# Optimization experiments

Hardware: AMD Instinct MI355X
Metric: run time of the kernel (lower is better)

The kernel has to match this reference:

```python
import jax, jax.numpy as jnp
import numpy as np

B, C, L = 32, 64, 2048
FREQ = L // 2 + 1            # 1025
BAND_SIZES = [341, 341, 343]  # freq//3, freq//3, remainder


def setup_inputs() -> dict:
    key = jax.random.key(0)
    k = jax.random.split(key, 6)
    X = jax.random.normal(k[0], (B, C, L), dtype=jnp.float32)
    A0 = jax.random.normal(k[1], (BAND_SIZES[0], BAND_SIZES[0]), dtype=jnp.float32)
    A1 = jax.random.normal(k[2], (BAND_SIZES[1], BAND_SIZES[1]), dtype=jnp.float32)
    A2 = jax.random.normal(k[3], (BAND_SIZES[2], BAND_SIZES[2]), dtype=jnp.float32)
    fusion_weights = jnp.ones((3,), dtype=jnp.float32)
    # Gumbel(0,1) noise for the 2-way gumbel-softmax over each (b, i, j) entry
    gumbel_noise = jax.random.gumbel(k[4], (B, C, C, 2), dtype=jnp.float32)
    return {"X": X, "A0": A0, "A1": A1, "A2": A2,
            "fusion_weights": fusion_weights, "gumbel_noise": gumbel_noise}


def _band_dist(band, A):
    # band: (b, c, s), A: (s, s). dist[b,i,j] = ||A (band_i - band_j)||^2
    # Gram trick: ||y_i - y_j||^2 = q_i + q_j - 2 y_i . y_j, y = band @ A^T
    Y = jnp.einsum('ds,bcs->bcd', A, band)          # (b, c, s)
    G = jnp.einsum('bid,bjd->bij', Y, Y)            # (b, c, c)
    q = jnp.einsum('bid,bid->bi', Y, Y)             # (b, c)
    dist = q[:, :, None] + q[:, None, :] - 2.0 * G
    return jnp.maximum(dist, 0.0)                   # guard fp round-off


def reference(X, A0, A1, A2, fusion_weights, gumbel_noise):
    XF = jnp.abs(jnp.fft.rfft(X, axis=-1))          # (b, c, FREQ)
    s0, s1, s2 = BAND_SIZES
    bands = (XF[..., :s0], XF[..., s0:s0 + s1], XF[..., s0 + s1:])
    As = (A0, A1, A2)
    dists = jnp.stack([_band_dist(b_, A_) for b_, A_ in zip(bands, As)], axis=-1)  # (b,c,c,3)
    w = jax.nn.softmax(fusion_weights)
    dist = jnp.einsum('bijk,k->bij', dists, w)      # (b, c, c)

    exp_dist = 1.0 / (dist + 1e-10)
    eye = jnp.eye(C, dtype=exp_dist.dtype)
    mask = 1.0 - eye
    exp_dist = exp_dist * mask
    exp_max = jax.lax.stop_gradient(jnp.max(exp_dist, axis=-1, keepdims=True))
    p = exp_dist / exp_max
    p = (p * mask + eye) * 0.99                     # probs in (0, 0.99]

    # Bernoulli via 2-class gumbel-softmax (hard, tau=1, straight-through)
    logits = jnp.stack([jnp.log(p / (1.0 - p)), jnp.log((1.0 - p) / p)], axis=-1)  # (b,c,c,2)
    y = logits + gumbel_noise
    y_soft = jax.nn.softmax(y, axis=-1)
    y_hard = jax.nn.one_hot(jnp.argmax(y, axis=-1), 2, dtype=y_soft.dtype)
    sample = (y_hard - jax.lax.stop_gradient(y_soft) + y_soft)[..., 0]  # (b,c,c)
    return sample[:, None, :, :]                    # (b, 1, c, c)
```

## Files before the change

kernel.cpp:

```cpp
#include <hip/hip_runtime.h>
#include <math.h>

#define Bn 32
#define Cn 64
#define Ln 2048
#define NFREQ 1025
#define S0c 341
#define S1c 341
#define S2c 343
#define KPAD 352
#define XROW (3 * 1056)
#define APLANE (3 * KPAD * KPAD)

#define PI_D 3.14159265358979323846

typedef double v4d __attribute__((ext_vector_type(4)));
typedef unsigned short u16;
typedef __attribute__((ext_vector_type(4))) u16 u16x4;
typedef __attribute__((ext_vector_type(8))) short short8;
typedef __attribute__((ext_vector_type(4))) float f32x4;

#define PADIX(i) ((i) + ((i) >> 4))

__device__ __forceinline__ u16 rneb(float f) {
    unsigned u = __float_as_uint(f);
    unsigned r = (u + 0x7FFFu + ((u >> 16) & 1u)) >> 16;
    return (u16)r;
}
__device__ __forceinline__ float b2f(u16 h) {
    return __uint_as_float(((unsigned)h) << 16);
}
__device__ __forceinline__ void split3(float v, u16& h1, u16& h2, u16& h3) {
    h1 = rneb(v);
    float r1 = v - b2f(h1);
    h2 = rneb(r1);
    float r2 = r1 - b2f(h2);
    h3 = rneb(r2);
}

__device__ __forceinline__ int rev4_10(unsigned x) {
    unsigned t = __brev(x) >> 22;
    return (int)(((t & 0x155u) << 1) | ((t >> 1) & 0x155u));
}

__global__ __launch_bounds__(256) void k_fftprep(const float* __restrict__ X,
                                                 const float* __restrict__ A0,
                                                 const float* __restrict__ A1,
                                                 const float* __restrict__ A2,
                                                 u16* __restrict__ XS,
                                                 u16* __restrict__ AS) {
    __shared__ float re[1088];
    __shared__ float im[1088];
    __shared__ float2 twl[2048];
    int blk = blockIdx.x;
    int tid = threadIdx.x;

    if (blk >= Bn * Cn) {
        int i = blk - Bn * Cn;
        int z = i / 484;
        const float* A = (z == 0) ? A0 : ((z == 1) ? A1 : A2);
        int S = (z == 2) ? S2c : S0c;
        int idx = (i % 484) * 256 + tid;
        int d = idx / KPAD, kk = idx - d * KPAD;
        float v = (d < S && kk < S) ? A[(size_t)d * S + kk] : 0.0f;
        u16 h1, h2, h3;
        split3(v, h1, h2, h3);
        size_t o = ((size_t)z * KPAD + d) * KPAD + kk;
        AS[o] = h1;
        AS[APLANE + o] = h2;
        AS[2 * (size_t)APLANE + o] = h3;
        return;
    }

    int row = blk;
    #pragma unroll
    for (int ii = 0; ii < 8; ++ii) {
        int t = tid + 256 * ii;
        float ang = (float)(-2.0 * PI_D / 2048.0 * (double)t);
        float s, c;
        sincosf(ang, &s, &c);
        twl[t] = make_float2(c, s);
    }
    __syncthreads();
    {
        int k = tid;
        float2 w1 = twl[2 * k];
        float2 w2 = twl[4 * k];
        float2 w3 = twl[6 * k];
        int i0 = PADIX(k), i1 = PADIX(k + 256), i2 = PADIX(k + 512), i3 = PADIX(k + 768);
        const float2* xr = (const float2*)(X + (size_t)row * Ln);
        float2 v0 = xr[k];
        float2 v1 = xr[k + 256];
        float2 v2 = xr[k + 512];
        float2 v3 = xr[k + 768];
        float ar = v0.x, ai = v0.y;
        float br = v1.x, bi = v1.y;
        float cr = v2.x, ci = v2.y;
        float dr = v3.x, di = v3.y;
        float t0r = ar + cr, t0i = ai + ci;
        float t1r = ar - cr, t1i = ai - ci;
        float t2r = br + dr, t2i = bi + di;
        float t3r = br - dr, t3i = bi - di;
        re[i0] = t0r + t2r; im[i0] = t0i + t2i;
        float u1r = t1r + t3i, u1i = t1i - t3r;
        re[i1] = u1r * w1.x - u1i * w1.y; im[i1] = u1r * w1.y + u1i * w1.x;
        float u2r = t0r - t2r, u2i = t0i - t2i;
        re[i2] = u2r * w2.x - u2i * w2.y; im[i2] = u2r * w2.y + u2i * w2.x;
        float u3r = t1r - t3i, u3i = t1i + t3r;
        re[i3] = u3r * w3.x - u3i * w3.y; im[i3] = u3r * w3.y + u3i * w3.x;
    }
    __syncthreads();
    #pragma unroll
    for (int s = 1; s < 5; ++s) {
        int log2Q = 8 - 2 * s;
        int Q = 1 << log2Q;
        int k = tid & (Q - 1);
        int g = tid >> log2Q;
        int base = (g << (log2Q + 2)) + k;
        int i0 = PADIX(base), i1 = PADIX(base + Q), i2 = PADIX(base + 2 * Q), i3 = PADIX(base + 3 * Q);
        int step = 2 << (2 * s);
        float2 w1 = twl[k * step];
        float2 w2 = twl[2 * k * step];
        float2 w3 = twl[3 * k * step];
        float ar = re[i0], ai = im[i0];
        float br = re[i1], bi = im[i1];
        float cr = re[i2], ci = im[i2];
        float dr = re[i3], di = im[i3];
        float t0r = ar + cr, t0i = ai + ci;
        float t1r = ar - cr, t1i = ai - ci;
        float t2r = br + dr, t2i = bi + di;
        float t3r = br - dr, t3i = bi - di;
        re[i0] = t0r + t2r; im[i0] = t0i + t2i;
        float u1r = t1r + t3i, u1i = t1i - t3r;
        re[i1] = u1r * w1.x - u1i * w1.y; im[i1] = u1r * w1.y + u1i * w1.x;
        float u2r = t0r - t2r, u2i = t0i - t2i;
        re[i2] = u2r * w2.x - u2i * w2.y; im[i2] = u2r * w2.y + u2i * w2.x;
        float u3r = t1r - t3i, u3i = t1i + t3r;
        re[i3] = u3r * w3.x - u3i * w3.y; im[i3] = u3r * w3.y + u3i * w3.x;
        __syncthreads();
    }
    u16* xrow = XS + (size_t)row * XROW;
    if (tid < 31) {
        int pp = (tid < 11) ? (341 + tid) : ((tid < 22) ? (682 + tid) : (1025 + tid));
        xrow[pp] = 0; xrow[1056 + pp] = 0; xrow[2112 + pp] = 0;
    }
    for (int k = tid; k <= 1024; k += 256) {
        float Xr, Xi;
        if (k == 0)        { Xr = re[0] + im[0]; Xi = 0.0f; }
        else if (k == 1024){ Xr = re[0] - im[0]; Xi = 0.0f; }
        else {
            int rv  = PADIX(rev4_10((unsigned)k));
            int rv2 = PADIX(rev4_10((unsigned)(1024 - k)));
            float2 t = twl[k];
            float Zr = re[rv],  Zi = im[rv];
            float Wr = re[rv2], Wi = im[rv2];
            float Er = 0.5f * (Zr + Wr), Ei = 0.5f * (Zi - Wi);
            float Or = 0.5f * (Zi + Wi), Oi = -0.5f * (Zr - Wr);
            Xr = Er + t.x * Or - t.y * Oi;
            Xi = Ei + t.x * Oi + t.y * Or;
        }
        float v = sqrtf(Xr * Xr + Xi * Xi);
        int zb = (k < S0c) ? 0 : ((k < S0c + S1c) ? 1 : 2);
        int pos = k + 11 * zb;
        u16 h1, h2, h3;
        split3(v, h1, h2, h3);
        xrow[pos] = h1;
        xrow[1056 + pos] = h2;
        xrow[2112 + pos] = h3;
    }
}

__global__ __launch_bounds__(256) void k_gemm(const u16* __restrict__ XS,
                                              const u16* __restrict__ AS,
                                              float* __restrict__ Y) {
    const int Sarr[3] = {S0c, S1c, S2c};
    const int Oarr[3] = {0, S0c, S0c + S1c};
    int z = blockIdx.z;
    int S = Sarr[z], O = Oarr[z];

    __shared__ u16 sX1[64][40], sX2[64][40], sX3[64][40];
    __shared__ u16 sA1[32][40], sA2[32][40], sA3[32][40];

    int r0 = blockIdx.x * 64;
    int d0 = blockIdx.y * 32;
    int tid = threadIdx.x;
    int lane = tid & 63, w = tid >> 6;
    int wm = (w >> 1) * 32, wn = (w & 1) * 16;
    int fm = lane & 15, kq = lane >> 4;
    int row8 = tid >> 3, seg4 = (tid & 7) * 4;

    f32x4 z4 = {0.0f, 0.0f, 0.0f, 0.0f};
    short8 aone, afm;
    {
        u16 hone = 0x3F80;
        u16 hfm = rneb((float)fm);
        #pragma unroll
        for (int j = 0; j < 8; ++j) { aone[j] = (short)hone; afm[j] = (short)hfm; }
    }
    f32x4 calR = __builtin_amdgcn_mfma_f32_16x16x32_bf16(afm, aone, z4, 0, 0, 0);
    f32x4 calC = __builtin_amdgcn_mfma_f32_16x16x32_bf16(aone, afm, z4, 0, 0, 0);
    int rIdx[4], cIdx[4];
    #pragma unroll
    for (int i = 0; i < 4; ++i) {
        rIdx[i] = (int)(calR[i] * 0.03125f + 0.5f);
        cIdx[i] = (int)(calC[i] * 0.03125f + 0.5f);
    }

    const u16* xb0 = XS + (size_t)(r0 + row8) * XROW + (size_t)z * KPAD + seg4;
    const u16* xb1 = xb0 + 32 * (size_t)XROW;
    const u16* ab  = AS + ((size_t)z * KPAD + (d0 + row8)) * KPAD + seg4;

    u16x4 wxa1, wxa2, wxa3, wxb1, wxb2, wxb3, wa1, wa2, wa3;
    auto load_tile = [&](int st) {
        int ko = st * 32;
        wxa1 = *(const u16x4*)(xb0 + ko);
        wxa2 = *(const u16x4*)(xb0 + 1056 + ko);
        wxa3 = *(const u16x4*)(xb0 + 2112 + ko);
        wxb1 = *(const u16x4*)(xb1 + ko);
        wxb2 = *(const u16x4*)(xb1 + 1056 + ko);
        wxb3 = *(const u16x4*)(xb1 + 2112 + ko);
        wa1  = *(const u16x4*)(ab + ko);
        wa2  = *(const u16x4*)(ab + APLANE + ko);
        wa3  = *(const u16x4*)(ab + 2 * (size_t)APLANE + ko);
    };

    double acc0[4] = {0.0, 0.0, 0.0, 0.0};
    double acc1[4] = {0.0, 0.0, 0.0, 0.0};
    load_tile(0);
    const int nsteps = KPAD / 32;
    for (int st = 0; st < nsteps; ++st) {
        __syncthreads();
        *(u16x4*)&sX1[row8][seg4] = wxa1;
        *(u16x4*)&sX2[row8][seg4] = wxa2;
        *(u16x4*)&sX3[row8][seg4] = wxa3;
        *(u16x4*)&sX1[row8 + 32][seg4] = wxb1;
        *(u16x4*)&sX2[row8 + 32][seg4] = wxb2;
        *(u16x4*)&sX3[row8 + 32][seg4] = wxb3;
        *(u16x4*)&sA1[row8][seg4] = wa1;
        *(u16x4*)&sA2[row8][seg4] = wa2;
        *(u16x4*)&sA3[row8][seg4] = wa3;
        __syncthreads();
        if (st + 1 < nsteps) load_tile(st + 1);
        short8 b1 = *(const short8*)&sA1[wn + fm][kq * 8];
        short8 b2 = *(const short8*)&sA2[wn + fm][kq * 8];
        short8 b3 = *(const short8*)&sA3[wn + fm][kq * 8];
        {
            short8 a1 = *(const short8*)&sX1[wm + fm][kq * 8];
            short8 a2 = *(const short8*)&sX2[wm + fm][kq * 8];
            short8 a3 = *(const short8*)&sX3[wm + fm][kq * 8];
            f32x4 p1 = __builtin_amdgcn_mfma_f32_16x16x32_bf16(a1, b1, z4, 0, 0, 0);
            f32x4 p2 = __builtin_amdgcn_mfma_f32_16x16x32_bf16(a1, b2, z4, 0, 0, 0);
            p2 = __builtin_amdgcn_mfma_f32_16x16x32_bf16(a2, b1, p2, 0, 0, 0);
            p2 = __builtin_amdgcn_mfma_f32_16x16x32_bf16(a1, b3, p2, 0, 0, 0);
            p2 = __builtin_amdgcn_mfma_f32_16x16x32_bf16(a2, b2, p2, 0, 0, 0);
            p2 = __builtin_amdgcn_mfma_f32_16x16x32_bf16(a3, b1, p2, 0, 0, 0);
            #pragma unroll
            for (int i = 0; i < 4; ++i) acc0[i] += (double)p1[i] + (double)p2[i];
        }
        {
            short8 a1 = *(const short8*)&sX1[wm + 16 + fm][kq * 8];
            short8 a2 = *(const short8*)&sX2[wm + 16 + fm][kq * 8];
            short8 a3 = *(const short8*)&sX3[wm + 16 + fm][kq * 8];
            f32x4 p1 = __builtin_amdgcn_mfma_f32_16x16x32_bf16(a1, b1, z4, 0, 0, 0);
            f32x4 p2 = __builtin_amdgcn_mfma_f32_16x16x32_bf16(a1, b2, z4, 0, 0, 0);
            p2 = __builtin_amdgcn_mfma_f32_16x16x32_bf16(a2, b1, p2, 0, 0, 0);
            p2 = __builtin_amdgcn_mfma_f32_16x16x32_bf16(a1, b3, p2, 0, 0, 0);
            p2 = __builtin_amdgcn_mfma_f32_16x16x32_bf16(a2, b2, p2, 0, 0, 0);
            p2 = __builtin_amdgcn_mfma_f32_16x16x32_bf16(a3, b1, p2, 0, 0, 0);
            #pragma unroll
            for (int i = 0; i < 4; ++i) acc1[i] += (double)p1[i] + (double)p2[i];
        }
    }
    #pragma unroll
    for (int i = 0; i < 4; ++i) {
        int d = d0 + wn + cIdx[i];
        if (d < S) {
            Y[(size_t)(r0 + wm + rIdx[i]) * NFREQ + O + d] = (float)acc0[i];
            Y[(size_t)(r0 + wm + 16 + rIdx[i]) * NFREQ + O + d] = (float)acc1[i];
        }
    }
}

__global__ __launch_bounds__(256) void k_dist(const float* __restrict__ Y,
                                              const float* __restrict__ fw,
                                              double* __restrict__ part) {
    __shared__ double sY[64][34];
    int b = blockIdx.x;
    int chunk = blockIdx.y;
    int dlo = chunk * 128;
    int dhi = (chunk == 7) ? NFREQ : dlo + 128;
    int tid = threadIdx.x;
    int lane = tid & 63, w = tid >> 6;
    int wm = (w >> 1) * 32, wn = (w & 1) * 32;
    int fm = lane & 15, kq = lane >> 4;
    int kl = tid & 31, rl = tid >> 5;

    double f0 = (double)fw[0], f1 = (double)fw[1], f2 = (double)fw[2];
    double m = fmax(f0, fmax(f1, f2));
    double e0 = exp(f0 - m), e1 = exp(f1 - m), e2 = exp(f2 - m);
    double esum = e0 + e1 + e2;
    double sw0 = sqrt(e0 / esum), sw1 = sqrt(e1 / esum), sw2 = sqrt(e2 / esum);

    v4d zero = {0.0, 0.0, 0.0, 0.0};
    double aval = (double)fm;
    v4d calR = __builtin_amdgcn_mfma_f64_16x16x4f64(aval, 1.0, zero, 0, 0, 0);
    v4d calC = __builtin_amdgcn_mfma_f64_16x16x4f64(1.0, aval, zero, 0, 0, 0);
    int rIdx[4], cIdx[4];
    #pragma unroll
    for (int i = 0; i < 4; ++i) {
        rIdx[i] = (int)(calR[i] * 0.25);
        cIdx[i] = (int)(calC[i] * 0.25);
    }

    const float* Yb = Y + (size_t)b * Cn * NFREQ;
    auto load_tile = [&](int k0, double* py) {
        int d = dlo + k0 + kl;
        bool dv = d < dhi;
        double sw = dv ? ((d < S0c) ? sw0 : ((d < S0c + S1c) ? sw1 : sw2)) : 0.0;
        #pragma unroll
        for (int i = 0; i < 8; ++i)
            py[i] = dv ? (double)Yb[(size_t)(rl + 8 * i) * NFREQ + d] * sw : 0.0;
    };

    v4d acc00 = zero, acc01 = zero, acc10 = zero, acc11 = zero;
    double py[8];
    load_tile(0, py);
    int nsteps = (dhi - dlo + 31) / 32;
    for (int st = 0; st < nsteps; ++st) {
        __syncthreads();
        #pragma unroll
        for (int i = 0; i < 8; ++i) sY[rl + 8 * i][kl] = py[i];
        __syncthreads();
        if (st + 1 < nsteps) load_tile((st + 1) * 32, py);
        #pragma unroll
        for (int t = 0; t < 8; ++t) {
            int k = 4 * t + kq;
            double a0 = sY[wm + fm][k];
            double a1 = sY[wm + 16 + fm][k];
            double b0 = sY[wn + fm][k];
            double b1 = sY[wn + 16 + fm][k];
            acc00 = __builtin_amdgcn_mfma_f64_16x16x4f64(a0, b0, acc00, 0, 0, 0);
            acc01 = __builtin_amdgcn_mfma_f64_16x16x4f64(a0, b1, acc01, 0, 0, 0);
            acc10 = __builtin_amdgcn_mfma_f64_16x16x4f64(a1, b0, acc10, 0, 0, 0);
            acc11 = __builtin_amdgcn_mfma_f64_16x16x4f64(a1, b1, acc11, 0, 0, 0);
        }
    }
    double* pb = part + (((size_t)b * 8 + chunk) << 12);
    #pragma unroll
    for (int i = 0; i < 4; ++i) {
        int rowA = wm + rIdx[i], rowB = rowA + 16;
        int cA = wn + cIdx[i], cB = cA + 16;
        pb[rowA * 64 + cA] = acc00[i];
        pb[rowA * 64 + cB] = acc01[i];
        pb[rowB * 64 + cA] = acc10[i];
        pb[rowB * 64 + cB] = acc11[i];
    }
}

__global__ __launch_bounds__(256) void k_decide(const double* __restrict__ part,
                                                const float* __restrict__ gum,
                                                float* __restrict__ out) {
    __shared__ double sQ[64];
    int b = blockIdx.x;
    int tid = threadIdx.x;
    const double* pb = part + (((size_t)b * 8) << 12);
    if (tid < 64) {
        double q = 0.0;
        #pragma unroll
        for (int c = 0; c < 8; ++c) q += pb[((size_t)c << 12) + tid * 65];
        sQ[tid] = q;
    }
    __syncthreads();
    int i = blockIdx.y * 4 + (tid >> 6);
    int j = tid & 63;
    double g = 0.0;
    #pragma unroll
    for (int c = 0; c < 8; ++c) g += pb[((size_t)c << 12) + i * 64 + j];
    double dist = fmax(sQ[i] + sQ[j] - 2.0 * g, 0.0);
    double e = (i == j) ? 0.0 : 1.0 / (dist + 1e-10);
    double emax = e;
    #pragma unroll
    for (int off = 32; off; off >>= 1)
        emax = fmax(emax, __shfl_xor(emax, off, 64));
    double p = (i == j) ? 0.99 : (e / emax) * 0.99;
    double l0 = log(p / (1.0 - p));
    double l1 = -l0;
    int idx = i * 64 + j;
    const float* gb = gum + (size_t)b * 8192;
    double y0 = l0 + (double)gb[2 * idx];
    double y1 = l1 + (double)gb[2 * idx + 1];
    out[(size_t)b * 4096 + idx] = (y0 >= y1) ? 1.0f : 0.0f;
}

extern "C" void kernel_launch(void* const* d_in, const int* in_sizes, int n_in,
                              void* d_out, int out_size, void* d_ws, size_t ws_size,
                              hipStream_t stream) {
    const float* X  = (const float*)d_in[0];
    const float* A0 = (const float*)d_in[1];
    const float* A1 = (const float*)d_in[2];
    const float* A2 = (const float*)d_in[3];
    const float* fw = (const float*)d_in[4];
    const float* gm = (const float*)d_in[5];
    float* out = (float*)d_out;

    char* ws = (char*)d_ws;
    u16*  XS = (u16*)(ws + 32768);
    u16*  AS = (u16*)(ws + 13008896);
    float* Y = (float*)(ws + 15239168);
    double* part = (double*)(ws + 32768);

    k_fftprep<<<Bn * Cn + 1452, 256, 0, stream>>>(X, A0, A1, A2, XS, AS);
    k_gemm<<<dim3(32, 11, 3), 256, 0, stream>>>(XS, AS, Y);
    k_dist<<<dim3(Bn, 8), 256, 0, stream>>>(Y, fw, part);
    k_decide<<<dim3(Bn, 16), 256, 0, stream>>>(part, gm, out);
}
```

Baseline: 134.3 us.

## Fuse decide stage into k_dist via last-block atomic counter per batch

```diff
diff --git a/kernel.cpp b/kernel.cpp
--- a/kernel.cpp
+++ b/kernel.cpp
@@ -48,7 +48,8 @@
                                                  const float* __restrict__ A1,
                                                  const float* __restrict__ A2,
                                                  u16* __restrict__ XS,
-                                                 u16* __restrict__ AS) {
+                                                 u16* __restrict__ AS,
+                                                 unsigned* __restrict__ cnt) {
     __shared__ float re[1088];
     __shared__ float im[1088];
     __shared__ float2 twl[2048];
@@ -57,6 +58,7 @@
 
     if (blk >= Bn * Cn) {
         int i = blk - Bn * Cn;
+        if (i == 0 && tid < Bn) cnt[tid] = 0;
         int z = i / 484;
         const float* A = (z == 0) ? A0 : ((z == 1) ? A1 : A2);
         int S = (z == 2) ? S2c : S0c;
@@ -283,8 +285,12 @@
 
 __global__ __launch_bounds__(256) void k_dist(const float* __restrict__ Y,
                                               const float* __restrict__ fw,
-                                              double* __restrict__ part) {
+                                              double* __restrict__ part,
+                                              unsigned* __restrict__ cnt,
+                                              const float* __restrict__ gum,
+                                              float* __restrict__ out) {
     __shared__ double sY[64][34];
+    __shared__ int isLast;
     int b = blockIdx.x;
     int chunk = blockIdx.y;
     int dlo = chunk * 128;
@@ -345,7 +351,8 @@
             acc11 = __builtin_amdgcn_mfma_f64_16x16x4f64(a1, b1, acc11, 0, 0, 0);
         }
     }
-    double* pb = part + (((size_t)b * 8 + chunk) << 12);
+    double* pb0 = part + (((size_t)b * 8) << 12);
+    double* pb = pb0 + ((size_t)chunk << 12);
     #pragma unroll
     for (int i = 0; i < 4; ++i) {
         int rowA = wm + rIdx[i], rowB = rowA + 16;
@@ -355,41 +362,43 @@
         pb[rowB * 64 + cA] = acc10[i];
         pb[rowB * 64 + cB] = acc11[i];
     }
-}
-
-__global__ __launch_bounds__(256) void k_decide(const double* __restrict__ part,
-                                                const float* __restrict__ gum,
-                                                float* __restrict__ out) {
+
+    __threadfence();
+    __syncthreads();
+    if (tid == 0) isLast = (atomicAdd(&cnt[b], 1u) == 7u);
+    __syncthreads();
+    if (!isLast) return;
+    __threadfence();
+
     __shared__ double sQ[64];
-    int b = blockIdx.x;
-    int tid = threadIdx.x;
-    const double* pb = part + (((size_t)b * 8) << 12);
     if (tid < 64) {
         double q = 0.0;
         #pragma unroll
-        for (int c = 0; c < 8; ++c) q += pb[((size_t)c << 12) + tid * 65];
+        for (int c = 0; c < 8; ++c) q += pb0[((size_t)c << 12) + tid * 65];
         sQ[tid] = q;
     }
     __syncthreads();
-    int i = blockIdx.y * 4 + (tid >> 6);
-    int j = tid & 63;
-    double g = 0.0;
-    #pragma unroll
-    for (int c = 0; c < 8; ++c) g += pb[((size_t)c << 12) + i * 64 + j];
-    double dist = fmax(sQ[i] + sQ[j] - 2.0 * g, 0.0);
-    double e = (i == j) ? 0.0 : 1.0 / (dist + 1e-10);
-    double emax = e;
-    #pragma unroll
-    for (int off = 32; off; off >>= 1)
-        emax = fmax(emax, __shfl_xor(emax, off, 64));
-    double p = (i == j) ? 0.99 : (e / emax) * 0.99;
-    double l0 = log(p / (1.0 - p));
-    double l1 = -l0;
-    int idx = i * 64 + j;
     const float* gb = gum + (size_t)b * 8192;
-    double y0 = l0 + (double)gb[2 * idx];
-    double y1 = l1 + (double)gb[2 * idx + 1];
-    out[(size_t)b * 4096 + idx] = (y0 >= y1) ? 1.0f : 0.0f;
+    float* ob = out + (size_t)b * 4096;
+    for (int pass = 0; pass < 16; ++pass) {
+        int i = pass * 4 + (tid >> 6);
+        int j = tid & 63;
+        double g = 0.0;
+        #pragma unroll
+        for (int c = 0; c < 8; ++c) g += pb0[((size_t)c << 12) + i * 64 + j];
+        double dist = fmax(sQ[i] + sQ[j] - 2.0 * g, 0.0);
+        double e = (i == j) ? 0.0 : 1.0 / (dist + 1e-10);
+        double emax = e;
+        #pragma unroll
+        for (int off = 32; off; off >>= 1)
+            emax = fmax(emax, __shfl_xor(emax, off, 64));
+        double p = (i == j) ? 0.99 : (e / emax) * 0.99;
+        double l0 = log(p / (1.0 - p));
+        int idx = i * 64 + j;
+        double y0 = l0 + (double)gb[2 * idx];
+        double y1 = -l0 + (double)gb[2 * idx + 1];
+        ob[idx] = (y0 >= y1) ? 1.0f : 0.0f;
+    }
 }
 
 extern "C" void kernel_launch(void* const* d_in, const int* in_sizes, int n_in,
@@ -404,13 +413,13 @@
     float* out = (float*)d_out;
 
     char* ws = (char*)d_ws;
+    unsigned* cnt = (unsigned*)(ws);
     u16*  XS = (u16*)(ws + 32768);
     u16*  AS = (u16*)(ws + 13008896);
     float* Y = (float*)(ws + 15239168);
     double* part = (double*)(ws + 32768);
 
-    k_fftprep<<<Bn * Cn + 1452, 256, 0, stream>>>(X, A0, A1, A2, XS, AS);
+    k_fftprep<<<Bn * Cn + 1452, 256, 0, stream>>>(X, A0, A1, A2, XS, AS, cnt);
     k_gemm<<<dim3(32, 11, 3), 256, 0, stream>>>(XS, AS, Y);
-    k_dist<<<dim3(Bn, 8), 256, 0, stream>>>(Y, fw, part);
-    k_decide<<<dim3(Bn, 16), 256, 0, stream>>>(part, gm, out);
-}
+    k_dist<<<dim3(Bn, 8), 256, 0, stream>>>(Y, fw, part, cnt, gm, out);
+}
```

Result: slower. 186.1 us (+38.6%).
